# Kernel tuning notes

Hardware: AMD Instinct MI355X
Metric: run time of the kernel (lower is better)

The kernel has to match this reference:

```python
import jax, jax.numpy as jnp
import numpy as np

B, S, D = 2, 2048, 2048
H = 16
HD = D // H  # 128


def setup_inputs() -> dict:
    key = jax.random.key(0)
    k1, k2, k3 = jax.random.split(key, 3)
    scale = 0.02
    return {
        "hidden_states": jax.random.normal(k1, (B, S, D), dtype=jnp.float32),
        "c_attn_w": jax.random.normal(k2, (D, 3 * D), dtype=jnp.float32) * scale,
        "c_attn_b": jnp.zeros((3 * D,), dtype=jnp.float32),
        "c_proj_w": jax.random.normal(k3, (D, D), dtype=jnp.float32) * scale,
        "c_proj_b": jnp.zeros((D,), dtype=jnp.float32),
    }


def reference(hidden_states, c_attn_w, c_attn_b, c_proj_w, c_proj_b):
    # Conv1D: x @ W + b  (W is [in, out])
    qkv = hidden_states @ c_attn_w + c_attn_b            # [B,S,3D]
    q, k, v = jnp.split(qkv, 3, axis=-1)                 # each [B,S,D]

    def split_heads(t):
        return t.reshape(B, S, H, HD).transpose(0, 2, 1, 3)  # [B,H,S,HD]

    q, k, v = split_heads(q), split_heads(k), split_heads(v)

    # scaled dot-product scores (scale_attn_weights=True)
    scores = jnp.einsum("bhqd,bhkd->bhqk", q, k) / jnp.sqrt(
        jnp.asarray(HD, dtype=q.dtype)
    )
    # causal mask (tril bias buffer)
    causal = jnp.tril(jnp.ones((S, S), dtype=bool))
    mask_value = jnp.finfo(scores.dtype).min
    scores = jnp.where(causal[None, None, :, :], scores, mask_value)

    attn = jax.nn.softmax(scores, axis=-1)               # [B,H,S,S]
    ctx = jnp.einsum("bhqk,bhkd->bhqd", attn, v)         # [B,H,S,HD]
    ctx = ctx.transpose(0, 2, 1, 3).reshape(B, S, D)      # merge heads

    out = ctx @ c_proj_w + c_proj_b                       # [B,S,D]
    return out
```

## Files before the change

kernel.cpp:

```cpp
#include <hip/hip_runtime.h>

typedef unsigned short u16;
typedef __bf16 bfx8 __attribute__((ext_vector_type(8)));
typedef float f32x4 __attribute__((ext_vector_type(4)));

#define B_ 2
#define S_ 2048
#define D_ 2048
#define H_ 16
#define HD_ 128
#define SD_ 6144

__device__ __forceinline__ u16 f2bf(float f) {
  union { float f; unsigned u; } v; v.f = f;
  unsigned r = v.u + 0x7fffu + ((v.u >> 16) & 1u);
  return (u16)(r >> 16);
}
__device__ __forceinline__ float bf2f(u16 b) {
  union { unsigned u; float f; } v; v.u = ((unsigned)b) << 16;
  return v.f;
}
__device__ __forceinline__ void gload_lds16(const void* g, void* l) {
  __builtin_amdgcn_global_load_lds((const __attribute__((address_space(1))) void*)g,
                                   (__attribute__((address_space(3))) void*)l, 16, 0, 0);
}

#define BAR() do { asm volatile("" ::: "memory"); __builtin_amdgcn_s_barrier(); \
                   asm volatile("" ::: "memory"); } while (0)
#define WAIT_VM4() asm volatile("s_waitcnt vmcnt(4)" ::: "memory")
#define WAIT_VM0() asm volatile("s_waitcnt vmcnt(0)" ::: "memory")

__global__ __launch_bounds__(256) void cvt_kernel(const float* __restrict__ in,
                                                  u16* __restrict__ out, int n4) {
  int i = blockIdx.x * blockDim.x + threadIdx.x;
  int stride = gridDim.x * blockDim.x;
  for (int idx = i; idx < n4; idx += stride) {
    float4 v = ((const float4*)in)[idx];
    uint2 o;
    o.x = (unsigned)f2bf(v.x) | ((unsigned)f2bf(v.y) << 16);
    o.y = (unsigned)f2bf(v.z) | ((unsigned)f2bf(v.w) << 16);
    ((uint2*)out)[idx] = o;
  }
}

__global__ __launch_bounds__(256) void transpose_cvt(const float* __restrict__ in,
                                                     u16* __restrict__ out,
                                                     int R, int C) {
  __shared__ float tile[32][33];
  int tx = threadIdx.x, ty = threadIdx.y;
  int c0 = blockIdx.x * 32, r0 = blockIdx.y * 32;
  for (int i = 0; i < 4; ++i)
    tile[ty + i * 8][tx] = in[(size_t)(r0 + ty + i * 8) * C + c0 + tx];
  __syncthreads();
  for (int i = 0; i < 4; ++i)
    out[(size_t)(c0 + ty + i * 8) * R + r0 + tx] = f2bf(tile[tx][ty + i * 8]);
}

__global__ __launch_bounds__(256) void transpose_v(const u16* __restrict__ qkv,
                                                   u16* __restrict__ vt) {
  __shared__ u16 tile[32][33];
  int tx = threadIdx.x, ty = threadIdx.y;
  int bh = blockIdx.z;
  int b = bh >> 4, h = bh & 15;
  int s0 = blockIdx.x * 32, d0 = blockIdx.y * 32;
  const u16* src = qkv + (size_t)b * S_ * SD_ + 2 * D_ + h * HD_;
  for (int i = 0; i < 4; ++i)
    tile[ty + i * 8][tx] = src[(size_t)(s0 + ty + i * 8) * SD_ + d0 + tx];
  __syncthreads();
  u16* dst = vt + (size_t)bh * HD_ * S_;
  for (int i = 0; i < 4; ++i)
    dst[(size_t)(d0 + ty + i * 8) * S_ + s0 + tx] = tile[tx][ty + i * 8];
}

template<int OUT_BF16>
__global__ __launch_bounds__(512, 2) void gemm8p(const u16* __restrict__ A,
                                                 const u16* __restrict__ Bt,
                                                 const float* __restrict__ bias,
                                                 void* __restrict__ Cout,
                                                 int M, int N, int K) {
  __shared__ u16 lds[2][2][2][256 * 32];

  int t = threadIdx.x, l = t & 63, w = t >> 6;
  int lr = l & 15, lg = l >> 4;
  int wr = w >> 2, wc = w & 3;

  int nwg = gridDim.x * gridDim.y;
  int flat = blockIdx.x + gridDim.x * blockIdx.y;
  int swz = (flat & 7) * (nwg >> 3) + (flat >> 3);
  int m0 = (swz / gridDim.x) * 256, n0 = (swz % gridDim.x) * 256;

  f32x4 acc[8][4];
#pragma unroll
  for (int i = 0; i < 8; ++i)
#pragma unroll
    for (int j = 0; j < 4; ++j)
#pragma unroll
      for (int r = 0; r < 4; ++r) acc[i][j][r] = 0.0f;

  int srow = t >> 2, sc = t & 3;
  const u16* As0 = A  + (size_t)(m0 + srow) * K + ((sc ^ ((srow >> 1) & 3)) * 8);
  const u16* Bs0 = Bt + (size_t)(n0 + srow) * K + ((sc ^ ((srow >> 1) & 3)) * 8);
  size_t hstep = (size_t)128 * K;

#define STG_A(BUF, KH, KOFF) do { \
    gload_lds16(As0 + (KOFF),         &lds[0][BUF][KH][t * 8]); \
    gload_lds16(As0 + hstep + (KOFF), &lds[0][BUF][KH][4096 + t * 8]); \
  } while (0)
#define STG_B(BUF, KH, KOFF) do { \
    gload_lds16(Bs0 + (KOFF),         &lds[1][BUF][KH][t * 8]); \
    gload_lds16(Bs0 + hstep + (KOFF), &lds[1][BUF][KH][4096 + t * 8]); \
  } while (0)

  int NT = K >> 6;
  int rsw = (lg ^ ((lr >> 1) & 3)) * 8;
  int arow = wr * 128 + lr;
  int brow = wc * 64 + lr;

  STG_A(0, 0, 0); STG_B(0, 0, 0); STG_A(0, 1, 32); STG_B(0, 1, 32);
  WAIT_VM4();
  BAR();

  for (int g = 0; g < NT; ++g) {
    int cb = g & 1, sb = cb ^ 1;
    int koff = (g + 1) * 64;
    bool stg = (g + 1 < NT);
    bfx8 af[4], bfr[4];

#pragma unroll
    for (int i = 0; i < 4; ++i)
      af[i] = *(const bfx8*)&lds[0][cb][0][(arow + i * 16) * 32 + rsw];
#pragma unroll
    for (int j = 0; j < 4; ++j)
      bfr[j] = *(const bfx8*)&lds[1][cb][0][(brow + j * 16) * 32 + rsw];
    if (stg) STG_A(sb, 0, koff);
    BAR();
    __builtin_amdgcn_s_setprio(1);
#pragma unroll
    for (int i = 0; i < 4; ++i)
#pragma unroll
      for (int j = 0; j < 4; ++j)
        acc[i][j] = __builtin_amdgcn_mfma_f32_16x16x32_bf16(af[i], bfr[j], acc[i][j], 0, 0, 0);
    __builtin_amdgcn_s_setprio(0);
    BAR();

#pragma unroll
    for (int i = 0; i < 4; ++i)
      af[i] = *(const bfx8*)&lds[0][cb][0][(arow + 64 + i * 16) * 32 + rsw];
    if (stg) STG_B(sb, 0, koff);
    BAR();
    __builtin_amdgcn_s_setprio(1);
#pragma unroll
    for (int i = 0; i < 4; ++i)
#pragma unroll
      for (int j = 0; j < 4; ++j)
        acc[4 + i][j] = __builtin_amdgcn_mfma_f32_16x16x32_bf16(af[i], bfr[j], acc[4 + i][j], 0, 0, 0);
    __builtin_amdgcn_s_setprio(0);
    if (stg) WAIT_VM4(); else WAIT_VM0();
    BAR();

#pragma unroll
    for (int i = 0; i < 4; ++i)
      af[i] = *(const bfx8*)&lds[0][cb][1][(arow + i * 16) * 32 + rsw];
#pragma unroll
    for (int j = 0; j < 4; ++j)
      bfr[j] = *(const bfx8*)&lds[1][cb][1][(brow + j * 16) * 32 + rsw];
    if (stg) STG_A(sb, 1, koff + 32);
    BAR();
    __builtin_amdgcn_s_setprio(1);
#pragma unroll
    for (int i = 0; i < 4; ++i)
#pragma unroll
      for (int j = 0; j < 4; ++j)
        acc[i][j] = __builtin_amdgcn_mfma_f32_16x16x32_bf16(af[i], bfr[j], acc[i][j], 0, 0, 0);
    __builtin_amdgcn_s_setprio(0);
    BAR();

#pragma unroll
    for (int i = 0; i < 4; ++i)
      af[i] = *(const bfx8*)&lds[0][cb][1][(arow + 64 + i * 16) * 32 + rsw];
    if (stg) STG_B(sb, 1, koff + 32);
    BAR();
    __builtin_amdgcn_s_setprio(1);
#pragma unroll
    for (int i = 0; i < 4; ++i)
#pragma unroll
      for (int j = 0; j < 4; ++j)
        acc[4 + i][j] = __builtin_amdgcn_mfma_f32_16x16x32_bf16(af[i], bfr[j], acc[4 + i][j], 0, 0, 0);
    __builtin_amdgcn_s_setprio(0);
    if (stg) WAIT_VM4();
    BAR();
  }
#undef STG_A
#undef STG_B

  for (int i = 0; i < 8; ++i) {
    int row = m0 + wr * 128 + i * 16 + lg * 4;
    for (int j = 0; j < 4; ++j) {
      int col = n0 + wc * 64 + j * 16 + lr;
      float bz = bias[col];
      for (int r = 0; r < 4; ++r) {
        float v = acc[i][j][r] + bz;
        if (OUT_BF16)
          ((u16*)Cout)[(size_t)(row + r) * N + col] = f2bf(v);
        else
          ((float*)Cout)[(size_t)(row + r) * N + col] = v;
      }
    }
  }
}

#define STAGE(BUF, KT) do {                                                        \
    int kc_ = ((t & 15) ^ ((t >> 4) & 7)) * 8;                                     \
    for (int i_ = 0; i_ < 4; ++i_)                                                 \
      gload_lds16(kbase + (size_t)((KT) * 64 + i_ * 16 + (t >> 4)) * SD_ + kc_,    \
                  &Klds[BUF][i_ * 2048 + t * 8]);                                  \
    int vc_ = (KT) * 64 + (((t & 7) ^ ((t >> 3) & 7)) * 8);                        \
    for (int i_ = 0; i_ < 4; ++i_)                                                 \
      gload_lds16(vbase + (size_t)(i_ * 32 + (t >> 3)) * S_ + vc_,                 \
                  &Vlds[BUF][i_ * 2048 + t * 8]);                                  \
  } while (0)

__global__ __launch_bounds__(256) void attn_kernel(const u16* __restrict__ qkv,
                                                   const u16* __restrict__ vt,
                                                   u16* __restrict__ ctx) {
  __shared__ u16 Klds[2][64 * 128];
  __shared__ u16 Vlds[2][128 * 64];
  __shared__ u16 Plds[4][16 * 64];

  int t = threadIdx.x, l = t & 63, w = t >> 6;
  int lr = l & 15, lg = l >> 4;
  int sw = lr & 7;
  int bid = blockIdx.x;
  int pr = bid >> 5, bh = bid & 31;
  int b = bh >> 4, h = bh & 15;
  const float scale = 0.08838834764831845f;

  const u16* kbase = qkv + (size_t)b * S_ * SD_ + D_ + h * HD_;
  const u16* vbase = vt + (size_t)bh * HD_ * S_;

  for (int sgi = 0; sgi < 2; ++sgi) {
    int qt = sgi ? pr : (31 - pr);
    int q0 = qt * 64;
    int wbase = q0 + w * 16;
    int nt = qt + 1;

    bfx8 qf[4];
    {
      const u16* qbase = qkv + (size_t)(b * S_ + wbase) * SD_ + h * HD_;
      for (int kk = 0; kk < 4; ++kk) {
        const u16* src = qbase + (size_t)lr * SD_ + kk * 32 + lg * 8;
        union { uint4 u; u16 s[8]; bfx8 bv; } iv, ov;
        iv.u = *(const uint4*)src;
        for (int j = 0; j < 8; ++j) ov.s[j] = f2bf(bf2f(iv.s[j]) * scale);
        qf[kk] = ov.bv;
      }
    }

    f32x4 o[8];
    float mrun = -INFINITY, lrun = 0.0f;
    for (int ht = 0; ht < 8; ++ht)
      for (int r = 0; r < 4; ++r) o[ht][r] = 0.0f;

    if (sgi) __syncthreads();
    STAGE(0, 0);

    for (int kt = 0; kt < nt; ++kt) {
      int cur = kt & 1;
      __syncthreads();
      if (kt + 1 < nt) STAGE(cur ^ 1, kt + 1);

      int kb0 = kt * 64;

      f32x4 sacc[4];
      for (int n = 0; n < 4; ++n)
        for (int r = 0; r < 4; ++r) sacc[n][r] = 0.0f;
      __builtin_amdgcn_s_setprio(1);
      for (int n = 0; n < 4; ++n) {
        bfx8 kf[4];
        int krow = n * 16 + lr;
        for (int kk = 0; kk < 4; ++kk)
          kf[kk] = *(const bfx8*)&Klds[cur][krow * 128 + ((kk * 4 + lg) ^ sw) * 8];
        for (int kk = 0; kk < 4; ++kk)
          sacc[n] = __builtin_amdgcn_mfma_f32_16x16x32_bf16(kf[kk], qf[kk], sacc[n], 0, 0, 0);
      }
      __builtin_amdgcn_s_setprio(0);

      int q = wbase + lr;
      if (kb0 + 63 > wbase) {
        for (int n = 0; n < 4; ++n)
          for (int r = 0; r < 4; ++r)
            if (kb0 + n * 16 + lg * 4 + r > q) sacc[n][r] = -INFINITY;
      }
      float tm = -INFINITY;
      for (int n = 0; n < 4; ++n) {
        float a = fmaxf(fmaxf(sacc[n][0], sacc[n][1]),
                        fmaxf(sacc[n][2], sacc[n][3]));
        tm = fmaxf(tm, a);
      }
      tm = fmaxf(tm, __shfl_xor(tm, 16, 64));
      tm = fmaxf(tm, __shfl_xor(tm, 32, 64));
      float mold = mrun;
      float mnew = fmaxf(mold, tm);
      if (__any((int)(mnew > mold))) {
        float corr = __expf(mold - mnew);
        lrun *= corr;
        mrun = mnew;
        for (int r = 0; r < 4; ++r) {
          float c = __shfl(corr, lg * 4 + r, 16);
          for (int ht = 0; ht < 8; ++ht) o[ht][r] *= c;
        }
      }
      float mm = mrun;
      float psum = 0.0f;
      for (int n = 0; n < 4; ++n) {
        float p0 = __expf(sacc[n][0] - mm);
        float p1 = __expf(sacc[n][1] - mm);
        float p2 = __expf(sacc[n][2] - mm);
        float p3 = __expf(sacc[n][3] - mm);
        psum += (p0 + p1) + (p2 + p3);
        uint2 pk;
        pk.x = (unsigned)f2bf(p0) | ((unsigned)f2bf(p1) << 16);
        pk.y = (unsigned)f2bf(p2) | ((unsigned)f2bf(p3) << 16);
        *(uint2*)&Plds[w][lr * 64 + ((n * 2 + (lg >> 1)) ^ sw) * 8 + (lg & 1) * 4] = pk;
      }
      psum += __shfl_xor(psum, 16, 64);
      psum += __shfl_xor(psum, 32, 64);
      lrun += psum;

      __builtin_amdgcn_s_setprio(1);
      for (int kk = 0; kk < 2; ++kk) {
        bfx8 pa = *(const bfx8*)&Plds[w][lr * 64 + ((kk * 4 + lg) ^ sw) * 8];
        for (int ht = 0; ht < 8; ++ht) {
          bfx8 vb = *(const bfx8*)&Vlds[cur][(ht * 16 + lr) * 64 + ((kk * 4 + lg) ^ sw) * 8];
          o[ht] = __builtin_amdgcn_mfma_f32_16x16x32_bf16(pa, vb, o[ht], 0, 0, 0);
        }
      }
      __builtin_amdgcn_s_setprio(0);
    }

    for (int r = 0; r < 4; ++r) {
      float inv = 1.0f / __shfl(lrun, lg * 4 + r, 16);
      int qa = wbase + lg * 4 + r;
      u16* dst = ctx + (size_t)(b * S_ + qa) * D_ + h * HD_;
      for (int ht = 0; ht < 8; ++ht)
        dst[ht * 16 + lr] = f2bf(o[ht][r] * inv);
    }
  }
}

extern "C" void kernel_launch(void* const* d_in, const int* in_sizes, int n_in,
                              void* d_out, int out_size, void* d_ws, size_t ws_size,
                              hipStream_t stream) {
  const float* hs     = (const float*)d_in[0];
  const float* w_attn = (const float*)d_in[1];
  const float* b_attn = (const float*)d_in[2];
  const float* w_proj = (const float*)d_in[3];
  const float* b_proj = (const float*)d_in[4];

  u16* Xb     = (u16*)d_ws;
  u16* Wqkvt  = Xb     + 8388608;
  u16* Wprojt = Wqkvt  + 12582912;
  u16* qkvb   = Wprojt + 4194304;
  u16* Vt     = qkvb   + 25165824;
  u16* ctxb   = Vt     + 8388608;

  cvt_kernel<<<2048, 256, 0, stream>>>(hs, Xb, (B_ * S_ * D_) / 4);
  transpose_cvt<<<dim3(192, 64), dim3(32, 8), 0, stream>>>(w_attn, Wqkvt, D_, 3 * D_);
  transpose_cvt<<<dim3(64, 64), dim3(32, 8), 0, stream>>>(w_proj, Wprojt, D_, D_);
  gemm8p<1><<<dim3(24, 16), 512, 0, stream>>>(Xb, Wqkvt, b_attn, qkvb, 4096, 6144, 2048);
  transpose_v<<<dim3(64, 4, 32), dim3(32, 8), 0, stream>>>(qkvb, Vt);
  attn_kernel<<<dim3(512), 256, 0, stream>>>(qkvb, Vt, ctxb);
  gemm8p<0><<<dim3(8, 16), 512, 0, stream>>>(ctxb, Wprojt, b_proj, d_out, 4096, 2048, 2048);
}
```

Before: 284.4 us.

## Shrink GEMM tile to 128x256 and simplify the k-loop pipeline

Halves the M tile of both projection GEMMs from 256 to 128 rows, doubling the workgroup count to better fill the GPU, especially for the output projection, which previously launched only 128 workgroups. The k-loop is restructured into two compute phases per 64-wide tile instead of four, staging the A and B halves together, with an adjusted vmcnt wait. In exchange, each tile reuses B over fewer rows, which raises global and LDS traffic per FLOP.

```diff
diff --git a/kernel.cpp b/kernel.cpp
--- a/kernel.cpp
+++ b/kernel.cpp
@@ -27,7 +27,7 @@
 
 #define BAR() do { asm volatile("" ::: "memory"); __builtin_amdgcn_s_barrier(); \
                    asm volatile("" ::: "memory"); } while (0)
-#define WAIT_VM4() asm volatile("s_waitcnt vmcnt(4)" ::: "memory")
+#define WAIT_VM3() asm volatile("s_waitcnt vmcnt(3)" ::: "memory")
 #define WAIT_VM0() asm volatile("s_waitcnt vmcnt(0)" ::: "memory")
 
 __global__ __launch_bounds__(256) void cvt_kernel(const float* __restrict__ in,
@@ -73,12 +73,13 @@
 }
 
 template<int OUT_BF16>
-__global__ __launch_bounds__(512, 2) void gemm8p(const u16* __restrict__ A,
+__global__ __launch_bounds__(512, 2) void gemm2p(const u16* __restrict__ A,
                                                  const u16* __restrict__ Bt,
                                                  const float* __restrict__ bias,
                                                  void* __restrict__ Cout,
                                                  int M, int N, int K) {
-  __shared__ u16 lds[2][2][2][256 * 32];
+  __shared__ u16 ldsA[2][2][128 * 32];
+  __shared__ u16 ldsB[2][2][256 * 32];
 
   int t = threadIdx.x, l = t & 63, w = t >> 6;
   int lr = l & 15, lg = l >> 4;
@@ -87,37 +88,36 @@
   int nwg = gridDim.x * gridDim.y;
   int flat = blockIdx.x + gridDim.x * blockIdx.y;
   int swz = (flat & 7) * (nwg >> 3) + (flat >> 3);
-  int m0 = (swz / gridDim.x) * 256, n0 = (swz % gridDim.x) * 256;
-
-  f32x4 acc[8][4];
-#pragma unroll
-  for (int i = 0; i < 8; ++i)
+  int m0 = (swz / gridDim.x) * 128, n0 = (swz % gridDim.x) * 256;
+
+  f32x4 acc[4][4];
+#pragma unroll
+  for (int i = 0; i < 4; ++i)
 #pragma unroll
     for (int j = 0; j < 4; ++j)
 #pragma unroll
       for (int r = 0; r < 4; ++r) acc[i][j][r] = 0.0f;
 
   int srow = t >> 2, sc = t & 3;
-  const u16* As0 = A  + (size_t)(m0 + srow) * K + ((sc ^ ((srow >> 1) & 3)) * 8);
-  const u16* Bs0 = Bt + (size_t)(n0 + srow) * K + ((sc ^ ((srow >> 1) & 3)) * 8);
+  int csw = (sc ^ ((srow >> 1) & 3)) * 8;
+  const u16* As0 = A  + (size_t)(m0 + srow) * K + csw;
+  const u16* Bs0 = Bt + (size_t)(n0 + srow) * K + csw;
   size_t hstep = (size_t)128 * K;
 
-#define STG_A(BUF, KH, KOFF) do { \
-    gload_lds16(As0 + (KOFF),         &lds[0][BUF][KH][t * 8]); \
-    gload_lds16(As0 + hstep + (KOFF), &lds[0][BUF][KH][4096 + t * 8]); \
-  } while (0)
+#define STG_A(BUF, KH, KOFF) \
+    gload_lds16(As0 + (KOFF), &ldsA[BUF][KH][t * 8])
 #define STG_B(BUF, KH, KOFF) do { \
-    gload_lds16(Bs0 + (KOFF),         &lds[1][BUF][KH][t * 8]); \
-    gload_lds16(Bs0 + hstep + (KOFF), &lds[1][BUF][KH][4096 + t * 8]); \
+    gload_lds16(Bs0 + (KOFF),         &ldsB[BUF][KH][t * 8]); \
+    gload_lds16(Bs0 + hstep + (KOFF), &ldsB[BUF][KH][4096 + t * 8]); \
   } while (0)
 
   int NT = K >> 6;
   int rsw = (lg ^ ((lr >> 1) & 3)) * 8;
-  int arow = wr * 128 + lr;
+  int arow = wr * 64 + lr;
   int brow = wc * 64 + lr;
 
   STG_A(0, 0, 0); STG_B(0, 0, 0); STG_A(0, 1, 32); STG_B(0, 1, 32);
-  WAIT_VM4();
+  WAIT_VM3();
   BAR();
 
   for (int g = 0; g < NT; ++g) {
@@ -128,11 +128,11 @@
 
 #pragma unroll
     for (int i = 0; i < 4; ++i)
-      af[i] = *(const bfx8*)&lds[0][cb][0][(arow + i * 16) * 32 + rsw];
+      af[i] = *(const bfx8*)&ldsA[cb][0][(arow + i * 16) * 32 + rsw];
 #pragma unroll
     for (int j = 0; j < 4; ++j)
-      bfr[j] = *(const bfx8*)&lds[1][cb][0][(brow + j * 16) * 32 + rsw];
-    if (stg) STG_A(sb, 0, koff);
+      bfr[j] = *(const bfx8*)&ldsB[cb][0][(brow + j * 16) * 32 + rsw];
+    if (stg) { STG_A(sb, 0, koff); STG_B(sb, 0, koff); }
     BAR();
     __builtin_amdgcn_s_setprio(1);
 #pragma unroll
@@ -141,30 +141,16 @@
       for (int j = 0; j < 4; ++j)
         acc[i][j] = __builtin_amdgcn_mfma_f32_16x16x32_bf16(af[i], bfr[j], acc[i][j], 0, 0, 0);
     __builtin_amdgcn_s_setprio(0);
+    if (stg) WAIT_VM3(); else WAIT_VM0();
     BAR();
 
 #pragma unroll
     for (int i = 0; i < 4; ++i)
-      af[i] = *(const bfx8*)&lds[0][cb][0][(arow + 64 + i * 16) * 32 + rsw];
-    if (stg) STG_B(sb, 0, koff);
-    BAR();
-    __builtin_amdgcn_s_setprio(1);
-#pragma unroll
-    for (int i = 0; i < 4; ++i)
-#pragma unroll
-      for (int j = 0; j < 4; ++j)
-        acc[4 + i][j] = __builtin_amdgcn_mfma_f32_16x16x32_bf16(af[i], bfr[j], acc[4 + i][j], 0, 0, 0);
-    __builtin_amdgcn_s_setprio(0);
-    if (stg) WAIT_VM4(); else WAIT_VM0();
-    BAR();
-
-#pragma unroll
-    for (int i = 0; i < 4; ++i)
-      af[i] = *(const bfx8*)&lds[0][cb][1][(arow + i * 16) * 32 + rsw];
+      af[i] = *(const bfx8*)&ldsA[cb][1][(arow + i * 16) * 32 + rsw];
 #pragma unroll
     for (int j = 0; j < 4; ++j)
-      bfr[j] = *(const bfx8*)&lds[1][cb][1][(brow + j * 16) * 32 + rsw];
-    if (stg) STG_A(sb, 1, koff + 32);
+      bfr[j] = *(const bfx8*)&ldsB[cb][1][(brow + j * 16) * 32 + rsw];
+    if (stg) { STG_A(sb, 1, koff + 32); STG_B(sb, 1, koff + 32); }
     BAR();
     __builtin_amdgcn_s_setprio(1);
 #pragma unroll
@@ -173,28 +159,14 @@
       for (int j = 0; j < 4; ++j)
         acc[i][j] = __builtin_amdgcn_mfma_f32_16x16x32_bf16(af[i], bfr[j], acc[i][j], 0, 0, 0);
     __builtin_amdgcn_s_setprio(0);
-    BAR();
-
-#pragma unroll
-    for (int i = 0; i < 4; ++i)
-      af[i] = *(const bfx8*)&lds[0][cb][1][(arow + 64 + i * 16) * 32 + rsw];
-    if (stg) STG_B(sb, 1, koff + 32);
-    BAR();
-    __builtin_amdgcn_s_setprio(1);
-#pragma unroll
-    for (int i = 0; i < 4; ++i)
-#pragma unroll
-      for (int j = 0; j < 4; ++j)
-        acc[4 + i][j] = __builtin_amdgcn_mfma_f32_16x16x32_bf16(af[i], bfr[j], acc[4 + i][j], 0, 0, 0);
-    __builtin_amdgcn_s_setprio(0);
-    if (stg) WAIT_VM4();
+    if (stg) WAIT_VM3();
     BAR();
   }
 #undef STG_A
 #undef STG_B
 
-  for (int i = 0; i < 8; ++i) {
-    int row = m0 + wr * 128 + i * 16 + lg * 4;
+  for (int i = 0; i < 4; ++i) {
+    int row = m0 + wr * 64 + i * 16 + lg * 4;
     for (int j = 0; j < 4; ++j) {
       int col = n0 + wc * 64 + j * 16 + lr;
       float bz = bias[col];
@@ -367,8 +339,8 @@
   cvt_kernel<<<2048, 256, 0, stream>>>(hs, Xb, (B_ * S_ * D_) / 4);
   transpose_cvt<<<dim3(192, 64), dim3(32, 8), 0, stream>>>(w_attn, Wqkvt, D_, 3 * D_);
   transpose_cvt<<<dim3(64, 64), dim3(32, 8), 0, stream>>>(w_proj, Wprojt, D_, D_);
-  gemm8p<1><<<dim3(24, 16), 512, 0, stream>>>(Xb, Wqkvt, b_attn, qkvb, 4096, 6144, 2048);
+  gemm2p<1><<<dim3(24, 32), 512, 0, stream>>>(Xb, Wqkvt, b_attn, qkvb, 4096, 6144, 2048);
   transpose_v<<<dim3(64, 4, 32), dim3(32, 8), 0, stream>>>(qkvb, Vt);
   attn_kernel<<<dim3(512), 256, 0, stream>>>(qkvb, Vt, ctxb);
-  gemm8p<0><<<dim3(8, 16), 512, 0, stream>>>(ctxb, Wprojt, b_proj, d_out, 4096, 2048, 2048);
-}
+  gemm2p<0><<<dim3(8, 32), 512, 0, stream>>>(ctxb, Wprojt, b_proj, d_out, 4096, 2048, 2048);
+}
```

Measured after the change: 286.8 us. About the same (+0.8%).

## Use 128x256 tile GEMM for output projection and XCD-aware tile mapping

Applied to the files above, without the earlier changes.

Adds a gemm2p kernel with 128x256 tiles (4x4 MFMA accumulators per wave) for the c_proj GEMM. The grid grows from 128 to 256 workgroups, so the 256 CUs are better filled instead of half-idle. Also replaces the block swizzle with a tile_coords mapping that groups M rows per XCD and pairs adjacent N tiles, intended to improve L2 locality; this changes the QKV GEMM mapping as well. Smaller tiles lower per-block arithmetic intensity and add global traffic.

```diff
diff --git a/kernel.cpp b/kernel.cpp
--- a/kernel.cpp
+++ b/kernel.cpp
@@ -28,7 +28,18 @@
 #define BAR() do { asm volatile("" ::: "memory"); __builtin_amdgcn_s_barrier(); \
                    asm volatile("" ::: "memory"); } while (0)
 #define WAIT_VM4() asm volatile("s_waitcnt vmcnt(4)" ::: "memory")
+#define WAIT_VM3() asm volatile("s_waitcnt vmcnt(3)" ::: "memory")
 #define WAIT_VM0() asm volatile("s_waitcnt vmcnt(0)" ::: "memory")
+
+__device__ __forceinline__ void tile_coords(int BM, int BN, int& m0, int& n0) {
+  int flat = blockIdx.x + gridDim.x * blockIdx.y;
+  int xcd = flat & 7, li = flat >> 3;
+  int MW = gridDim.y >> 3;
+  int half = li >> 1, nn = li & 1;
+  int mloc = half % MW, nw = half / MW;
+  m0 = (xcd * MW + mloc) * BM;
+  n0 = (nw * 2 + nn) * BN;
+}
 
 __global__ __launch_bounds__(256) void cvt_kernel(const float* __restrict__ in,
                                                   u16* __restrict__ out, int n4) {
@@ -84,10 +95,8 @@
   int lr = l & 15, lg = l >> 4;
   int wr = w >> 2, wc = w & 3;
 
-  int nwg = gridDim.x * gridDim.y;
-  int flat = blockIdx.x + gridDim.x * blockIdx.y;
-  int swz = (flat & 7) * (nwg >> 3) + (flat >> 3);
-  int m0 = (swz / gridDim.x) * 256, n0 = (swz % gridDim.x) * 256;
+  int m0, n0;
+  tile_coords(256, 256, m0, n0);
 
   f32x4 acc[8][4];
 #pragma unroll
@@ -195,6 +204,113 @@
 
   for (int i = 0; i < 8; ++i) {
     int row = m0 + wr * 128 + i * 16 + lg * 4;
+    for (int j = 0; j < 4; ++j) {
+      int col = n0 + wc * 64 + j * 16 + lr;
+      float bz = bias[col];
+      for (int r = 0; r < 4; ++r) {
+        float v = acc[i][j][r] + bz;
+        if (OUT_BF16)
+          ((u16*)Cout)[(size_t)(row + r) * N + col] = f2bf(v);
+        else
+          ((float*)Cout)[(size_t)(row + r) * N + col] = v;
+      }
+    }
+  }
+}
+
+template<int OUT_BF16>
+__global__ __launch_bounds__(512, 2) void gemm2p(const u16* __restrict__ A,
+                                                 const u16* __restrict__ Bt,
+                                                 const float* __restrict__ bias,
+                                                 void* __restrict__ Cout,
+                                                 int M, int N, int K) {
+  __shared__ u16 ldsA[2][2][128 * 32];
+  __shared__ u16 ldsB[2][2][256 * 32];
+
+  int t = threadIdx.x, l = t & 63, w = t >> 6;
+  int lr = l & 15, lg = l >> 4;
+  int wr = w >> 2, wc = w & 3;
+
+  int m0, n0;
+  tile_coords(128, 256, m0, n0);
+
+  f32x4 acc[4][4];
+#pragma unroll
+  for (int i = 0; i < 4; ++i)
+#pragma unroll
+    for (int j = 0; j < 4; ++j)
+#pragma unroll
+      for (int r = 0; r < 4; ++r) acc[i][j][r] = 0.0f;
+
+  int srow = t >> 2, sc = t & 3;
+  int csw = (sc ^ ((srow >> 1) & 3)) * 8;
+  const u16* As0 = A  + (size_t)(m0 + srow) * K + csw;
+  const u16* Bs0 = Bt + (size_t)(n0 + srow) * K + csw;
+  size_t hstep = (size_t)128 * K;
+
+#define STG_A(BUF, KH, KOFF) \
+    gload_lds16(As0 + (KOFF), &ldsA[BUF][KH][t * 8])
+#define STG_B(BUF, KH, KOFF) do { \
+    gload_lds16(Bs0 + (KOFF),         &ldsB[BUF][KH][t * 8]); \
+    gload_lds16(Bs0 + hstep + (KOFF), &ldsB[BUF][KH][4096 + t * 8]); \
+  } while (0)
+
+  int NT = K >> 6;
+  int rsw = (lg ^ ((lr >> 1) & 3)) * 8;
+  int arow = wr * 64 + lr;
+  int brow = wc * 64 + lr;
+
+  STG_A(0, 0, 0); STG_B(0, 0, 0); STG_A(0, 1, 32); STG_B(0, 1, 32);
+  WAIT_VM3();
+  BAR();
+
+  for (int g = 0; g < NT; ++g) {
+    int cb = g & 1, sb = cb ^ 1;
+    int koff = (g + 1) * 64;
+    bool stg = (g + 1 < NT);
+    bfx8 af[4], bfr[4];
+
+#pragma unroll
+    for (int i = 0; i < 4; ++i)
+      af[i] = *(const bfx8*)&ldsA[cb][0][(arow + i * 16) * 32 + rsw];
+#pragma unroll
+    for (int j = 0; j < 4; ++j)
+      bfr[j] = *(const bfx8*)&ldsB[cb][0][(brow + j * 16) * 32 + rsw];
+    if (stg) { STG_A(sb, 0, koff); STG_B(sb, 0, koff); }
+    BAR();
+    __builtin_amdgcn_s_setprio(1);
+#pragma unroll
+    for (int i = 0; i < 4; ++i)
+#pragma unroll
+      for (int j = 0; j < 4; ++j)
+        acc[i][j] = __builtin_amdgcn_mfma_f32_16x16x32_bf16(af[i], bfr[j], acc[i][j], 0, 0, 0);
+    __builtin_amdgcn_s_setprio(0);
+    if (stg) WAIT_VM3(); else WAIT_VM0();
+    BAR();
+
+#pragma unroll
+    for (int i = 0; i < 4; ++i)
+      af[i] = *(const bfx8*)&ldsA[cb][1][(arow + i * 16) * 32 + rsw];
+#pragma unroll
+    for (int j = 0; j < 4; ++j)
+      bfr[j] = *(const bfx8*)&ldsB[cb][1][(brow + j * 16) * 32 + rsw];
+    if (stg) { STG_A(sb, 1, koff + 32); STG_B(sb, 1, koff + 32); }
+    BAR();
+    __builtin_amdgcn_s_setprio(1);
+#pragma unroll
+    for (int i = 0; i < 4; ++i)
+#pragma unroll
+      for (int j = 0; j < 4; ++j)
+        acc[i][j] = __builtin_amdgcn_mfma_f32_16x16x32_bf16(af[i], bfr[j], acc[i][j], 0, 0, 0);
+    __builtin_amdgcn_s_setprio(0);
+    if (stg) WAIT_VM3();
+    BAR();
+  }
+#undef STG_A
+#undef STG_B
+
+  for (int i = 0; i < 4; ++i) {
+    int row = m0 + wr * 64 + i * 16 + lg * 4;
     for (int j = 0; j < 4; ++j) {
       int col = n0 + wc * 64 + j * 16 + lr;
       float bz = bias[col];
@@ -370,5 +486,5 @@
   gemm8p<1><<<dim3(24, 16), 512, 0, stream>>>(Xb, Wqkvt, b_attn, qkvb, 4096, 6144, 2048);
   transpose_v<<<dim3(64, 4, 32), dim3(32, 8), 0, stream>>>(qkvb, Vt);
   attn_kernel<<<dim3(512), 256, 0, stream>>>(qkvb, Vt, ctxb);
-  gemm8p<0><<<dim3(8, 16), 512, 0, stream>>>(ctxb, Wprojt, b_proj, d_out, 4096, 2048, 2048);
-}
+  gemm2p<0><<<dim3(8, 32), 512, 0, stream>>>(ctxb, Wprojt, b_proj, d_out, 4096, 2048, 2048);
+}
```

New measurement: 269.3 us. 5.3% less time.
